# Optimization experiments

Hardware: AMD Instinct MI355X
Metric: run time of the kernel (lower is better)

The kernel has to match this reference:

```python
import math
import jax, jax.numpy as jnp
import numpy as np

B, N, C, H = 8, 512, 1024, 16
HD = C // H


def setup_inputs() -> dict:
    key = jax.random.key(0)
    ks = jax.random.split(key, 10)
    s = 0.02
    return {
        "x": jax.random.normal(ks[0], (B, N, C), jnp.float32),
        "mu": jax.random.normal(ks[1], (B, N, C), jnp.float32),
        "logvar": jax.random.normal(ks[2], (B, N, C), jnp.float32) * 0.1,
        "alpha": jax.random.uniform(ks[3], (B, N, 1), jnp.float32, 0.05, 1.0),
        "pi": jax.random.uniform(ks[4], (B, N, 1), jnp.float32, 0.05, 1.0),
        "z": jax.random.normal(ks[5], (B, N, C), jnp.float32),
        "w_q": jax.random.normal(ks[6], (C, C), jnp.float32) * s,
        "w_k": jax.random.normal(ks[7], (C, C), jnp.float32) * s,
        "w_v": jax.random.normal(ks[8], (C, C), jnp.float32) * s,
        "w_p": jax.random.normal(ks[9], (C, C), jnp.float32) * s,
        "b_p": jnp.zeros((C,), jnp.float32),
    }


def reference(x, mu, logvar, alpha, pi, z, w_q, w_k, w_v, w_p, b_p):
    # Non-meta NVIB path (set_mata_training_mode=False, qkv_bias=False).
    sqrt_hd = math.sqrt(HD)
    q = x @ w_q.T                                   # (B,N,C)
    biased_var = jnp.exp(logvar) + sqrt_hd          # (B,Nl,C)
    k = (mu / biased_var) @ w_k.T                   # (B,Nl,C)
    v = (sqrt_hd / biased_var * mu) @ w_v.T         # (B,Nl,C)

    def split_heads(t):
        b, n, _ = t.shape
        return t.reshape(b, n, H, HD).transpose(0, 2, 1, 3)  # (B,H,n,HD)

    qh, kh, vh = split_heads(q), split_heads(k), split_heads(v)
    attn = jnp.einsum("bhnd,bhmd->bhnm", qh, kh)    # (B,H,N,Nl)
    # additive log-alpha minus L2-norm bias, broadcast over heads and queries
    l2 = 0.5 * jnp.sum((mu / jnp.sqrt(biased_var)) ** 2, axis=-1)  # (B,Nl)
    bias = jnp.log(alpha[..., 0]) - l2              # (B,Nl)
    attn = attn + bias[:, None, None, :]
    attn = jax.nn.softmax(attn, axis=-1)
    out = jnp.einsum("bhnm,bhmd->bhnd", attn, vh)   # (B,H,N,HD)
    out = out.transpose(0, 2, 1, 3).reshape(x.shape[0], x.shape[1], C)
    out = out @ w_p.T + b_p
    return (out, attn)
```

## Files before the change

### kernel.cpp

```cpp
#include <hip/hip_runtime.h>
#include <hip/hip_bf16.h>

#define B_  8
#define N_  512
#define C_  1024
#define H_  16
#define HD_ 64
#define M_  4096

typedef float  f32x4  __attribute__((ext_vector_type(4)));
typedef __bf16 bf16x8 __attribute__((ext_vector_type(8)));
typedef unsigned short ushort_t;

__device__ __forceinline__ ushort_t f2bf(float f) {
  union { float f; unsigned int u; } un; un.f = f;
  unsigned int u = un.u;
  return (ushort_t)((u + 0x7fffu + ((u >> 16) & 1u)) >> 16);
}

__device__ __forceinline__ void gload16(const void* g, void* l) {
  __builtin_amdgcn_global_load_lds((const __attribute__((address_space(1))) void*)g,
                                   (__attribute__((address_space(3))) void*)l, 16, 0, 0);
}
#define SBAR()  __builtin_amdgcn_s_barrier()
#define SCHED() __builtin_amdgcn_sched_barrier(0)
#define VMCNT4() asm volatile("s_waitcnt vmcnt(4)" ::: "memory")
#define VMCNT0() asm volatile("s_waitcnt vmcnt(0)" ::: "memory")


__global__ __launch_bounds__(256) void prep_pack_kernel(
    const float* __restrict__ x, const float* __restrict__ mu,
    const float* __restrict__ logvar,
    const float* __restrict__ wq, const float* __restrict__ wk,
    const float* __restrict__ wv, const float* __restrict__ wp,
    ushort_t* __restrict__ xb, ushort_t* __restrict__ kp, ushort_t* __restrict__ vp,
    ushort_t* __restrict__ wb, float* __restrict__ l2part) {
  const int bid = blockIdx.x, t = threadIdx.x;
  const int row = t >> 1, cg = (t & 1) * 16;
  const int c0 = cg >> 3;

  if (bid < 1024) {
    const int mt = bid >> 5, kt = bid & 31;
    const size_t src = (size_t)(mt * 128 + row) * 1024 + kt * 32 + cg;
    ushort_t tx[16] __attribute__((aligned(16)));
    ushort_t tk[16] __attribute__((aligned(16)));
    ushort_t tv[16] __attribute__((aligned(16)));
    float l2 = 0.f;
#pragma unroll
    for (int j = 0; j < 4; ++j) {
      float4 xv = *(const float4*)(x + src + j * 4);
      float4 mv = *(const float4*)(mu + src + j * 4);
      float4 lv = *(const float4*)(logvar + src + j * 4);
      float xa[4] = {xv.x, xv.y, xv.z, xv.w};
      float ma[4] = {mv.x, mv.y, mv.z, mv.w};
      float la[4] = {lv.x, lv.y, lv.z, lv.w};
#pragma unroll
      for (int i = 0; i < 4; ++i) {
        int e = j * 4 + i;
        float bv  = __expf(la[i]) + 8.0f;
        float inv = 1.0f / bv;
        float kf  = ma[i] * inv;
        l2 += ma[i] * kf;
        tx[e] = f2bf(xa[i]); tk[e] = f2bf(kf); tv[e] = f2bf(8.0f * kf);
      }
    }
    const size_t tb = (size_t)((mt * 32 + kt) * 4) * 1024 + row * 8;
    *(bf16x8*)(xb + tb + c0 * 1024)       = *(const bf16x8*)(tx);
    *(bf16x8*)(xb + tb + (c0 + 1) * 1024) = *(const bf16x8*)(tx + 8);
    *(bf16x8*)(kp + tb + c0 * 1024)       = *(const bf16x8*)(tk);
    *(bf16x8*)(kp + tb + (c0 + 1) * 1024) = *(const bf16x8*)(tk + 8);
    *(bf16x8*)(vp + tb + c0 * 1024)       = *(const bf16x8*)(tv);
    *(bf16x8*)(vp + tb + (c0 + 1) * 1024) = *(const bf16x8*)(tv + 8);
    l2 += __shfl_xor(l2, 1);
    if ((t & 1) == 0) l2part[(size_t)(mt * 128 + row) * 32 + kt] = l2;
  } else {
    const int idx = bid - 1024;
    const int sel = idx >> 8, nt = (idx >> 5) & 7, kt = idx & 31;
    const float* src = sel == 0 ? wq : sel == 1 ? wk : sel == 2 ? wv : wp;
    const size_t so = (size_t)(nt * 128 + row) * 1024 + kt * 32 + cg;
    ushort_t tw[16] __attribute__((aligned(16)));
#pragma unroll
    for (int j = 0; j < 4; ++j) {
      float4 v = *(const float4*)(src + so + j * 4);
      tw[j * 4 + 0] = f2bf(v.x); tw[j * 4 + 1] = f2bf(v.y);
      tw[j * 4 + 2] = f2bf(v.z); tw[j * 4 + 3] = f2bf(v.w);
    }
    ushort_t* dst = wb + (size_t)sel * 1048576;
    const size_t tb = (size_t)((nt * 32 + kt) * 4) * 1024 + row * 8;
    *(bf16x8*)(dst + tb + c0 * 1024)       = *(const bf16x8*)(tw);
    *(bf16x8*)(dst + tb + (c0 + 1) * 1024) = *(const bf16x8*)(tw + 8);
  }
}

__device__ __forceinline__ void gemm_tile_r3(const ushort_t* __restrict__ Ag,
                                             const ushort_t* __restrict__ Wg,
                                             int amt, int ant, f32x4 acc[4][4],
                                             ushort_t* lds) {
  const int t = threadIdx.x;
  const int w = t >> 6, lane = t & 63;
  const int wm = w >> 1, wn = w & 1;
  const int chunk = lane >> 4, r15 = lane & 15;
  const int s0 = t, s1 = t + 256;

#define RSTAGE(kt, buf)                                                           \
  do {                                                                            \
    const ushort_t* sa = Ag + (size_t)(amt * 32 + (kt)) * 4096;                   \
    const ushort_t* sb = Wg + (size_t)(ant * 32 + (kt)) * 4096;                   \
    gload16(sa + s0 * 8, lds + (buf) * 4096 + (s0 & ~63) * 8);                    \
    gload16(sa + s1 * 8, lds + (buf) * 4096 + (s1 & ~63) * 8);                    \
    gload16(sb + s0 * 8, lds + 12288 + (buf) * 4096 + (s0 & ~63) * 8);            \
    gload16(sb + s1 * 8, lds + 12288 + (buf) * 4096 + (s1 & ~63) * 8);            \
  } while (0)

#define RCOMPUTE(j)                                                               \
  do {                                                                            \
    const ushort_t* Ab = lds + (j) * 4096;                                        \
    const ushort_t* Bb = lds + 12288 + (j) * 4096;                                \
    bf16x8 af[4], bw[4];                                                          \
    _Pragma("unroll")                                                             \
    for (int mi = 0; mi < 4; ++mi)                                                \
      af[mi] = *(const bf16x8*)(Ab + (chunk * 128 + wm * 64 + mi * 16 + r15) * 8);\
    _Pragma("unroll")                                                             \
    for (int ni = 0; ni < 4; ++ni)                                                \
      bw[ni] = *(const bf16x8*)(Bb + (chunk * 128 + wn * 64 + ni * 16 + r15) * 8);\
    __builtin_amdgcn_s_setprio(1);                                                \
    _Pragma("unroll")                                                             \
    for (int mi = 0; mi < 4; ++mi)                                                \
      _Pragma("unroll")                                                           \
      for (int ni = 0; ni < 4; ++ni)                                              \
        acc[mi][ni] = __builtin_amdgcn_mfma_f32_16x16x32_bf16(af[mi], bw[ni],     \
                                                              acc[mi][ni], 0, 0, 0); \
    __builtin_amdgcn_s_setprio(0);                                                \
    SCHED();                                                                      \
  } while (0)

  RSTAGE(0, 0); RSTAGE(1, 1);
  VMCNT4();
  SBAR(); SCHED();
  for (int kt0 = 0; kt0 < 30; kt0 += 3) {
    RSTAGE(kt0 + 2, 2); RCOMPUTE(0); VMCNT4(); SBAR(); SCHED();
    RSTAGE(kt0 + 3, 0); RCOMPUTE(1); VMCNT4(); SBAR(); SCHED();
    RSTAGE(kt0 + 4, 1); RCOMPUTE(2); VMCNT4(); SBAR(); SCHED();
  }
  RCOMPUTE(0); VMCNT0(); SBAR(); SCHED();
  RCOMPUTE(1);
#undef RSTAGE
#undef RCOMPUTE
}

__global__ __launch_bounds__(256, 3) void gemm_qkv_kernel(
    const ushort_t* __restrict__ xb, const ushort_t* __restrict__ kp,
    const ushort_t* __restrict__ vp, const ushort_t* __restrict__ wb,
    const float* __restrict__ alpha, const float* __restrict__ l2part,
    float* __restrict__ biasv,
    ushort_t* __restrict__ Qhs, ushort_t* __restrict__ Khs, ushort_t* __restrict__ Vts) {
  __shared__ ushort_t lds[24576];
  const int z = blockIdx.z;
  const ushort_t* Ag = z == 0 ? xb : z == 1 ? kp : vp;
  const ushort_t* Wg = wb + (size_t)z * 1048576;
  const int m0 = blockIdx.x * 128, n0 = blockIdx.y * 128;
  const int t = threadIdx.x;

  if (z == 0 && blockIdx.y == 0 && t < 128) {
    int row = m0 + t;
    const float* p = l2part + (size_t)row * 32;
    float s = 0.f;
#pragma unroll
    for (int j = 0; j < 8; ++j) {
      float4 v = *(const float4*)(p + j * 4);
      s += (v.x + v.y) + (v.z + v.w);
    }
    biasv[row] = __logf(alpha[row]) - 0.5f * s;
  }

  f32x4 acc[4][4] = {};
  gemm_tile_r3(Ag, Wg, blockIdx.x, blockIdx.y, acc, lds);
  const int w = t >> 6, lane = t & 63;
  const int wm = w >> 1, wn = w & 1;
  const int hi = lane >> 4, r15 = lane & 15;
  const int b = m0 >> 9, h0 = n0 >> 6;

  __syncthreads();
  if (z < 2) {
    ushort_t* T = lds;
#pragma unroll
    for (int mi = 0; mi < 4; ++mi)
#pragma unroll
      for (int ni = 0; ni < 4; ++ni)
#pragma unroll
        for (int q = 0; q < 4; ++q) {
          int row = wm * 64 + mi * 16 + hi * 4 + q;
          int col = wn * 64 + ni * 16 + r15;
          T[row * 136 + col] = f2bf(acc[mi][ni][q]);
        }
    __syncthreads();
    if (z == 0) {
      const int qt0 = (m0 & 511) >> 6;
#pragma unroll
      for (int i = 0; i < 8; ++i) {
        int c = t + 256 * i;
        int row64 = c & 63, qt_l = (c >> 6) & 1, chunk = (c >> 7) & 7, head_l = (c >> 10) & 1;
        bf16x8 v = *(const bf16x8*)(T + (qt_l * 64 + row64) * 136 + head_l * 64 + chunk * 8);
        int bh = b * 16 + h0 + head_l;
        *(bf16x8*)(Qhs + ((size_t)((bh * 8 + qt0 + qt_l) * 8 + chunk) * 64 + row64) * 8) = v;
      }
    } else {
      const int kt = (m0 & 511) >> 7;
#pragma unroll
      for (int i = 0; i < 8; ++i) {
        int c = t + 256 * i;
        int row128 = c & 127, chunk = (c >> 7) & 7, head_l = (c >> 10) & 1;
        bf16x8 v = *(const bf16x8*)(T + row128 * 136 + head_l * 64 + chunk * 8);
        int bh = b * 16 + h0 + head_l;
        *(bf16x8*)(Khs + ((size_t)((bh * 4 + kt) * 8 + chunk) * 128 + row128) * 8) = v;
      }
    }
  } else {
    ushort_t* T = lds;
#pragma unroll
    for (int mi = 0; mi < 4; ++mi)
#pragma unroll
      for (int ni = 0; ni < 4; ++ni)
#pragma unroll
        for (int q = 0; q < 4; ++q) {
          int row = wm * 64 + mi * 16 + hi * 4 + q;
          int col = wn * 64 + ni * 16 + r15;
          T[row * 129 + col] = f2bf(acc[mi][ni][q]);
        }
    __syncthreads();
    const int kt = (m0 & 511) >> 7;
#pragma unroll
    for (int i = 0; i < 8; ++i) {
      int c = t + 256 * i;
      int d64 = c & 63, head_l = (c >> 6) & 1, chunkp = (c >> 7) & 15;
      bf16x8 v;
#pragma unroll
      for (int j = 0; j < 8; ++j)
        v[j] = *(const __bf16*)(T + (chunkp * 8 + j) * 129 + head_l * 64 + d64);
      int bh = b * 16 + h0 + head_l;
      *(bf16x8*)(Vts + ((size_t)((bh * 4 + kt) * 16 + chunkp) * 64 + d64) * 8) = v;
    }
  }
}

__global__ __launch_bounds__(256, 2) void attn_kernel(
    const ushort_t* __restrict__ Qhs, const ushort_t* __restrict__ Khs,
    const ushort_t* __restrict__ Vts, const float* __restrict__ biasv,
    float* __restrict__ attn_out, ushort_t* __restrict__ Og) {
  __shared__ ushort_t Qt[4096];
  __shared__ ushort_t KV[16384];
  __shared__ ushort_t Pl[8192];
  __shared__ float biasl[512];
  const int bh = blockIdx.x, qt = blockIdx.y;
  const int b = bh >> 4, h = bh & 15;
  const int t = threadIdx.x, w = t >> 6, lane = t & 63;
  const int hi = lane >> 4, r15 = lane & 15;

  {
    float2 bv2 = *(const float2*)(biasv + b * 512 + t * 2);
    biasl[t * 2] = bv2.x; biasl[t * 2 + 1] = bv2.y;
  }
  {
    const ushort_t* sq = Qhs + (size_t)(bh * 8 + qt) * 4096;
    gload16(sq + t * 8, Qt + (t & ~63) * 8);
    gload16(sq + (t + 256) * 8, Qt + ((t + 256) & ~63) * 8);
  }

#define STAGE_K(kt, buf)                                                               \
  do {                                                                                 \
    const ushort_t* sk = Khs + (size_t)(bh * 4 + (kt)) * 8192;                         \
    _Pragma("unroll")                                                                  \
    for (int r = 0; r < 4; ++r) {                                                      \
      int s = r * 256 + t;                                                             \
      gload16(sk + s * 8, KV + (buf) * 8192 + (s & ~63) * 8);                          \
    }                                                                                  \
  } while (0)
#define STAGE_V(kt, buf)                                                               \
  do {                                                                                 \
    const ushort_t* sv = Vts + (size_t)(bh * 4 + (kt)) * 8192;                         \
    _Pragma("unroll")                                                                  \
    for (int r = 0; r < 4; ++r) {                                                      \
      int s = r * 256 + t;                                                             \
      gload16(sv + s * 8, KV + (buf) * 8192 + (s & ~63) * 8);                          \
    }                                                                                  \
  } while (0)

  STAGE_K(0, 0);
  f32x4 acc[32] = {};
  bf16x8 aq[2];
  int cur = 0;

#pragma unroll
  for (int kt = 0; kt < 4; ++kt) {
    if (kt < 3) STAGE_K(kt + 1, cur ^ 1);
    else        STAGE_V(0, cur ^ 1);
    VMCNT4();
    SBAR();
    SCHED();
    if (kt == 0) {
#pragma unroll
      for (int ks = 0; ks < 2; ++ks)
        aq[ks] = *(const bf16x8*)(Qt + ((ks * 4 + hi) * 64 + w * 16 + r15) * 8);
    }
    __builtin_amdgcn_s_setprio(1);
#pragma unroll
    for (int mf = 0; mf < 8; ++mf)
#pragma unroll
      for (int ks = 0; ks < 2; ++ks) {
        bf16x8 bk = *(const bf16x8*)(KV + cur * 8192 + ((ks * 4 + hi) * 128 + mf * 16 + r15) * 8);
        acc[kt * 8 + mf] = __builtin_amdgcn_mfma_f32_16x16x32_bf16(aq[ks], bk, acc[kt * 8 + mf], 0, 0, 0);
      }
    __builtin_amdgcn_s_setprio(0);
    SCHED();
    SBAR();
    SCHED();
    cur ^= 1;
  }

  float mx[4] = {-1e30f, -1e30f, -1e30f, -1e30f};
#pragma unroll
  for (int f = 0; f < 32; ++f) {
    float bv = biasl[f * 16 + r15];
#pragma unroll
    for (int q = 0; q < 4; ++q) {
      acc[f][q] += bv;
      mx[q] = fmaxf(mx[q], acc[f][q]);
    }
  }
#pragma unroll
  for (int q = 0; q < 4; ++q) {
    mx[q] = fmaxf(mx[q], __shfl_xor(mx[q], 1));
    mx[q] = fmaxf(mx[q], __shfl_xor(mx[q], 2));
    mx[q] = fmaxf(mx[q], __shfl_xor(mx[q], 4));
    mx[q] = fmaxf(mx[q], __shfl_xor(mx[q], 8));
  }
  float sm[4] = {0.f, 0.f, 0.f, 0.f};
#pragma unroll
  for (int f = 0; f < 32; ++f)
#pragma unroll
    for (int q = 0; q < 4; ++q) {
      float p = __expf(acc[f][q] - mx[q]);
      acc[f][q] = p;
      sm[q] += p;
    }
#pragma unroll
  for (int q = 0; q < 4; ++q) {
    sm[q] += __shfl_xor(sm[q], 1);
    sm[q] += __shfl_xor(sm[q], 2);
    sm[q] += __shfl_xor(sm[q], 4);
    sm[q] += __shfl_xor(sm[q], 8);
    sm[q] = 1.0f / sm[q];
  }
#pragma unroll
  for (int f = 0; f < 32; ++f)
#pragma unroll
    for (int q = 0; q < 4; ++q)
      acc[f][q] *= sm[q];

  f32x4 oacc[4] = {};
#pragma unroll
  for (int kt = 0; kt < 4; ++kt) {
    if (kt < 3) STAGE_V(kt + 1, cur ^ 1);
#pragma unroll
    for (int fl = 0; fl < 8; ++fl) {
      int f = kt * 8 + fl;
      int chunkp = fl * 2 + (r15 >> 3);
#pragma unroll
      for (int q = 0; q < 4; ++q)
        Pl[w * 2048 + (chunkp * 16 + hi * 4 + q) * 8 + (lane & 7)] = f2bf(acc[f][q]);
    }
    if (kt < 3) VMCNT4(); else VMCNT0();
    SBAR();
    SCHED();
    __builtin_amdgcn_s_setprio(1);
#pragma unroll
    for (int ks = 0; ks < 4; ++ks) {
      bf16x8 pa = *(const bf16x8*)(Pl + w * 2048 + ((ks * 4 + hi) * 16 + r15) * 8);
#pragma unroll
      for (int df = 0; df < 4; ++df) {
        bf16x8 vb = *(const bf16x8*)(KV + cur * 8192 + ((ks * 4 + hi) * 64 + df * 16 + r15) * 8);
        oacc[df] = __builtin_amdgcn_mfma_f32_16x16x32_bf16(pa, vb, oacc[df], 0, 0, 0);
      }
    }
    __builtin_amdgcn_s_setprio(0);
    SCHED();
    SBAR();
    SCHED();
    cur ^= 1;
  }

  float* ao = attn_out + ((size_t)bh * 512 + qt * 64 + w * 16 + hi * 4) * 512 + r15;
#pragma unroll
  for (int f = 0; f < 32; ++f)
#pragma unroll
    for (int q = 0; q < 4; ++q)
      ao[(size_t)q * 512 + f * 16] = acc[f][q];

  {
    const int mtile = b * 4 + (qt >> 1);
    const int rowl = (qt & 1) * 64 + w * 16 + hi * 4;
#pragma unroll
    for (int df = 0; df < 4; ++df) {
      int kto = h * 2 + (df >> 1);
      int chunko = (df & 1) * 2 + (r15 >> 3);
      size_t ob = ((size_t)((mtile * 32 + kto) * 4 + chunko) * 1024 + (r15 & 7));
#pragma unroll
      for (int q = 0; q < 4; ++q)
        Og[ob + (size_t)(rowl + q) * 8] = f2bf(oacc[df][q]);
    }
  }
#undef STAGE_K
#undef STAGE_V
}

__global__ __launch_bounds__(256, 3) void gemm_out_kernel(
    const ushort_t* __restrict__ Og, const ushort_t* __restrict__ wb,
    const float* __restrict__ bp, float* __restrict__ out) {
  __shared__ ushort_t lds[24576];
  const int m0 = blockIdx.x * 128, n0 = blockIdx.y * 128;
  f32x4 acc[4][4] = {};
  gemm_tile_r3(Og, wb + 3 * 1048576, blockIdx.x, blockIdx.y, acc, lds);
  const int t = threadIdx.x, w = t >> 6, lane = t & 63;
  const int wm = w >> 1, wn = w & 1;
  const int hi = lane >> 4, r15 = lane & 15;
  float* T2 = (float*)lds;
#pragma unroll
  for (int hh = 0; hh < 2; ++hh) {
    __syncthreads();
    if (wm == hh) {
#pragma unroll
      for (int mi = 0; mi < 4; ++mi)
#pragma unroll
        for (int ni = 0; ni < 4; ++ni)
#pragma unroll
          for (int q = 0; q < 4; ++q) {
            int row = mi * 16 + hi * 4 + q;
            int col = wn * 64 + ni * 16 + r15;
            T2[row * 128 + col] = acc[mi][ni][q];
          }
    }
    __syncthreads();
#pragma unroll
    for (int i = 0; i < 8; ++i) {
      int c = t + 256 * i;
      int row = c >> 5, col0 = (c & 31) * 4;
      float4 v = *(const float4*)(T2 + row * 128 + col0);
      float4 bb = *(const float4*)(bp + n0 + col0);
      v.x += bb.x; v.y += bb.y; v.z += bb.z; v.w += bb.w;
      *(float4*)(out + (size_t)(m0 + hh * 64 + row) * 1024 + n0 + col0) = v;
    }
  }
}

extern "C" void kernel_launch(void* const* d_in, const int* in_sizes, int n_in,
                              void* d_out, int out_size, void* d_ws, size_t ws_size,
                              hipStream_t stream) {
  const float* x      = (const float*)d_in[0];
  const float* mu     = (const float*)d_in[1];
  const float* logvar = (const float*)d_in[2];
  const float* alpha  = (const float*)d_in[3];
  const float* wq = (const float*)d_in[6];
  const float* wk = (const float*)d_in[7];
  const float* wv = (const float*)d_in[8];
  const float* wp = (const float*)d_in[9];
  const float* bp = (const float*)d_in[10];

  float* out      = (float*)d_out;
  float* attn_out = out + (size_t)M_ * C_;

  char* ws = (char*)d_ws;
  ushort_t* xb     = (ushort_t*)(ws);
  ushort_t* kp     = (ushort_t*)(ws + (size_t)8  * 1048576);
  ushort_t* vp     = (ushort_t*)(ws + (size_t)16 * 1048576);
  ushort_t* Qhs    = (ushort_t*)(ws + (size_t)24 * 1048576);
  ushort_t* Khs    = (ushort_t*)(ws + (size_t)32 * 1048576);
  ushort_t* Vts    = (ushort_t*)(ws + (size_t)40 * 1048576);
  ushort_t* wb     = (ushort_t*)(ws + (size_t)48 * 1048576);
  float*    biasv  = (float*)   (ws + (size_t)56 * 1048576);
  float*    l2part = (float*)   (ws + (size_t)57 * 1048576);
  ushort_t* Og     = xb;

  prep_pack_kernel<<<2048, 256, 0, stream>>>(x, mu, logvar, wq, wk, wv, wp,
                                             xb, kp, vp, wb, l2part);
  gemm_qkv_kernel<<<dim3(32, 8, 3), 256, 0, stream>>>(xb, kp, vp, wb,
                                                      alpha, l2part, biasv,
                                                      Qhs, Khs, Vts);
  attn_kernel<<<dim3(128, 8), 256, 0, stream>>>(Qhs, Khs, Vts, biasv, attn_out, Og);
  gemm_out_kernel<<<dim3(32, 8), 256, 0, stream>>>(Og, wb, bp, out);
}
```

Measured before the change: 110.0 us.

## Transpose QK MFMA output so each lane holds one query row

Swaps the MFMA operand order so the score accumulator is transposed: each lane now holds four consecutive key columns for a single query row. The softmax max and sum reductions then need only two cross-lane shuffles instead of sixteen, the bias is read as a vector, and the attention-probability writes to global memory become 16-byte vector stores. The shared-memory P buffer is re-laid out with a padded row stride (136) so the bf16 probabilities are written as 8-byte stores and read back as MFMA A fragments. The trade-off is a slightly larger LDS footprint and a changed bank-access pattern for P.

```diff
diff --git a/kernel.cpp b/kernel.cpp
--- a/kernel.cpp
+++ b/kernel.cpp
@@ -249,7 +249,7 @@
     float* __restrict__ attn_out, ushort_t* __restrict__ Og) {
   __shared__ ushort_t Qt[4096];
   __shared__ ushort_t KV[16384];
-  __shared__ ushort_t Pl[8192];
+  __shared__ ushort_t Pl[8704];
   __shared__ float biasl[512];
   const int bh = blockIdx.x, qt = blockIdx.y;
   const int b = bh >> 4, h = bh & 15;
@@ -308,7 +308,7 @@
 #pragma unroll
       for (int ks = 0; ks < 2; ++ks) {
         bf16x8 bk = *(const bf16x8*)(KV + cur * 8192 + ((ks * 4 + hi) * 128 + mf * 16 + r15) * 8);
-        acc[kt * 8 + mf] = __builtin_amdgcn_mfma_f32_16x16x32_bf16(aq[ks], bk, acc[kt * 8 + mf], 0, 0, 0);
+        acc[kt * 8 + mf] = __builtin_amdgcn_mfma_f32_16x16x32_bf16(bk, aq[ks], acc[kt * 8 + mf], 0, 0, 0);
       }
     __builtin_amdgcn_s_setprio(0);
     SCHED();
@@ -317,46 +317,36 @@
     cur ^= 1;
   }
 
-  float mx[4] = {-1e30f, -1e30f, -1e30f, -1e30f};
+  float mx = -1e30f;
 #pragma unroll
   for (int f = 0; f < 32; ++f) {
-    float bv = biasl[f * 16 + r15];
+    f32x4 bv4 = *(const f32x4*)(biasl + f * 16 + hi * 4);
+    acc[f] += bv4;
+    float m01 = fmaxf(acc[f][0], acc[f][1]);
+    float m23 = fmaxf(acc[f][2], acc[f][3]);
+    mx = fmaxf(mx, fmaxf(m01, m23));
+  }
+  mx = fmaxf(mx, __shfl_xor(mx, 16));
+  mx = fmaxf(mx, __shfl_xor(mx, 32));
+  float sm = 0.f;
+#pragma unroll
+  for (int f = 0; f < 32; ++f)
 #pragma unroll
     for (int q = 0; q < 4; ++q) {
-      acc[f][q] += bv;
-      mx[q] = fmaxf(mx[q], acc[f][q]);
-    }
-  }
-#pragma unroll
-  for (int q = 0; q < 4; ++q) {
-    mx[q] = fmaxf(mx[q], __shfl_xor(mx[q], 1));
-    mx[q] = fmaxf(mx[q], __shfl_xor(mx[q], 2));
-    mx[q] = fmaxf(mx[q], __shfl_xor(mx[q], 4));
-    mx[q] = fmaxf(mx[q], __shfl_xor(mx[q], 8));
-  }
-  float sm[4] = {0.f, 0.f, 0.f, 0.f};
+      float p = __expf(acc[f][q] - mx);
+      acc[f][q] = p;
+      sm += p;
+    }
+  sm += __shfl_xor(sm, 16);
+  sm += __shfl_xor(sm, 32);
+  float inv = 1.0f / sm;
 #pragma unroll
   for (int f = 0; f < 32; ++f)
 #pragma unroll
-    for (int q = 0; q < 4; ++q) {
-      float p = __expf(acc[f][q] - mx[q]);
-      acc[f][q] = p;
-      sm[q] += p;
-    }
-#pragma unroll
-  for (int q = 0; q < 4; ++q) {
-    sm[q] += __shfl_xor(sm[q], 1);
-    sm[q] += __shfl_xor(sm[q], 2);
-    sm[q] += __shfl_xor(sm[q], 4);
-    sm[q] += __shfl_xor(sm[q], 8);
-    sm[q] = 1.0f / sm[q];
-  }
-#pragma unroll
-  for (int f = 0; f < 32; ++f)
-#pragma unroll
     for (int q = 0; q < 4; ++q)
-      acc[f][q] *= sm[q];
-
+      acc[f][q] *= inv;
+
+  ushort_t* Plw = Pl + w * 2176;
   f32x4 oacc[4] = {};
 #pragma unroll
   for (int kt = 0; kt < 4; ++kt) {
@@ -364,10 +354,10 @@
 #pragma unroll
     for (int fl = 0; fl < 8; ++fl) {
       int f = kt * 8 + fl;
-      int chunkp = fl * 2 + (r15 >> 3);
-#pragma unroll
-      for (int q = 0; q < 4; ++q)
-        Pl[w * 2048 + (chunkp * 16 + hi * 4 + q) * 8 + (lane & 7)] = f2bf(acc[f][q]);
+      ushort4 o;
+      o.x = f2bf(acc[f][0]); o.y = f2bf(acc[f][1]);
+      o.z = f2bf(acc[f][2]); o.w = f2bf(acc[f][3]);
+      *(ushort4*)(Plw + r15 * 136 + fl * 16 + hi * 4) = o;
     }
     if (kt < 3) VMCNT4(); else VMCNT0();
     SBAR();
@@ -375,7 +365,7 @@
     __builtin_amdgcn_s_setprio(1);
 #pragma unroll
     for (int ks = 0; ks < 4; ++ks) {
-      bf16x8 pa = *(const bf16x8*)(Pl + w * 2048 + ((ks * 4 + hi) * 16 + r15) * 8);
+      bf16x8 pa = *(const bf16x8*)(Plw + r15 * 136 + ks * 32 + hi * 8);
 #pragma unroll
       for (int df = 0; df < 4; ++df) {
         bf16x8 vb = *(const bf16x8*)(KV + cur * 8192 + ((ks * 4 + hi) * 64 + df * 16 + r15) * 8);
@@ -389,12 +379,12 @@
     cur ^= 1;
   }
 
-  float* ao = attn_out + ((size_t)bh * 512 + qt * 64 + w * 16 + hi * 4) * 512 + r15;
-#pragma unroll
-  for (int f = 0; f < 32; ++f)
-#pragma unroll
-    for (int q = 0; q < 4; ++q)
-      ao[(size_t)q * 512 + f * 16] = acc[f][q];
+  {
+    float* ao = attn_out + ((size_t)bh * 512 + qt * 64 + w * 16 + r15) * 512 + hi * 4;
+#pragma unroll
+    for (int f = 0; f < 32; ++f)
+      *(f32x4*)(ao + f * 16) = acc[f];
+  }
 
   {
     const int mtile = b * 4 + (qt >> 1);
```

After: 110.4 us. Within noise of the previous version (+0.4%).
